# Kernel tuning notes

Measured on AMD Instinct MI355X. Metric: run time of the kernel, lower is better.

The kernel has to match this reference:

```python
import jax, jax.numpy as jnp
import numpy as np

DIM = 1024
HEADS = 16
EPS = 1e-5  # torch nn.LayerNorm default


def layernorm(x, g, b):
    # normalize over last axis
    mu = jnp.mean(x, axis=-1, keepdims=True)
    var = jnp.mean(jnp.square(x - mu), axis=-1, keepdims=True)
    return (x - mu) * jax.lax.rsqrt(var + EPS) * g + b


def setup_inputs() -> dict:
    key = jax.random.key(0)
    ks = jax.random.split(key, 8)
    B, N, C = 4, 1024, DIM
    s = 1.0 / np.sqrt(C)
    return {
        "x": jax.random.normal(ks[0], (B, N, C), jnp.float32),
        "qkv_w": jax.random.normal(ks[1], (3 * C, C), jnp.float32) * s,
        "qkv_b": jnp.zeros((3 * C,), jnp.float32),
        "q_norm_g": jnp.ones((C,), jnp.float32),
        "q_norm_b": jnp.zeros((C,), jnp.float32),
        "k_norm_g": jnp.ones((C,), jnp.float32),
        "k_norm_b": jnp.zeros((C,), jnp.float32),
        "proj_w": jax.random.normal(ks[2], (C, C), jnp.float32) * s,
        "proj_b": jnp.zeros((C,), jnp.float32),
    }


def reference(x, qkv_w, qkv_b, q_norm_g, q_norm_b, k_norm_g, k_norm_b, proj_w, proj_b):
    B, N, C = x.shape
    H = HEADS
    D = C // H
    scale = D ** -0.5

    qkv = x @ qkv_w.T + qkv_b                      # [B,N,3C]
    qkv = qkv.reshape(B, N, 3, H, D)
    q, k, v = qkv[:, :, 0], qkv[:, :, 1], qkv[:, :, 2]  # [B,N,H,D]

    # qk_normalization: LayerNorm over flattened (H*D)=C per token
    q = layernorm(q.reshape(B, N, C), q_norm_g, q_norm_b).reshape(B, N, H, D)
    k = layernorm(k.reshape(B, N, C), k_norm_g, k_norm_b).reshape(B, N, H, D)

    # attention: [B,H,N,N]
    attn = jnp.einsum('bqhd,bkhd->bhqk', q * scale, k)
    attn = jax.nn.softmax(attn, axis=-1)
    out = jnp.einsum('bhqk,bkhd->bqhd', attn, v).reshape(B, N, C)
    return out @ proj_w.T + proj_b
```

## Files before the change

### kernel.cpp

```cpp
#include <hip/hip_runtime.h>
#include <hip/hip_bf16.h>

#define C_DIM 1024
#define HEADS 16

typedef __bf16 bf16x8 __attribute__((ext_vector_type(8)));
typedef float f32x4 __attribute__((ext_vector_type(4)));

static __device__ __forceinline__ unsigned short f2bf(float f) {
  unsigned int u = __builtin_bit_cast(unsigned int, f);
  u += 0x7FFFu + ((u >> 16) & 1u);
  return (unsigned short)(u >> 16);
}

static __device__ __forceinline__ float bf2f(unsigned short u) {
  unsigned int v = ((unsigned int)u) << 16;
  return __builtin_bit_cast(float, v);
}

static __device__ __forceinline__ void glds16(const unsigned short* g,
                                              unsigned short* l) {
  __builtin_amdgcn_global_load_lds(
      (const __attribute__((address_space(1))) unsigned int*)g,
      (__attribute__((address_space(3))) unsigned int*)l, 16, 0, 0);
}

__global__ void cast_bf16_kernel(const float* __restrict__ src,
                                 unsigned short* __restrict__ dst, int n4) {
  int i = blockIdx.x * blockDim.x + threadIdx.x;
  if (i >= n4) return;
  float4 v = *reinterpret_cast<const float4*>(src + (size_t)i * 4);
  ushort4 o;
  o.x = f2bf(v.x); o.y = f2bf(v.y); o.z = f2bf(v.z); o.w = f2bf(v.w);
  *reinterpret_cast<ushort4*>(dst + (size_t)i * 4) = o;
}

__global__ void cast2_kernel(const float* __restrict__ s0,
                             const float* __restrict__ s1,
                             unsigned short* __restrict__ d0,
                             unsigned short* __restrict__ d1, int n40) {
  int i = blockIdx.x * 256 + threadIdx.x;
  const float* s;
  unsigned short* d;
  if (i < n40) { s = s0; d = d0; }
  else { s = s1; d = d1; i -= n40; }
  float4 v = *reinterpret_cast<const float4*>(s + (size_t)i * 4);
  ushort4 o;
  o.x = f2bf(v.x); o.y = f2bf(v.y); o.z = f2bf(v.z); o.w = f2bf(v.w);
  *reinterpret_cast<ushort4*>(d + (size_t)i * 4) = o;
}

template <bool BF16_OUT>
__global__ __launch_bounds__(256, 2) void gemm_nt(
    const unsigned short* __restrict__ A, const unsigned short* __restrict__ B,
    const float* __restrict__ bias, void* __restrict__ Cout,
    int M, int N, int K) {
  __shared__ __align__(16) unsigned short As[128 * 64];
  __shared__ __align__(16) unsigned short Bs[128 * 64];
  const int tid = threadIdx.x;
  const int lane = tid & 63;
  const int wave = tid >> 6;
  const int wm = wave >> 1, wn = wave & 1;
  const int g = lane >> 4, r = lane & 15;
  const int bm = blockIdx.x * 128, bn = blockIdx.y * 128;

  f32x4 acc[4][4] = {};

  for (int k0 = 0; k0 < K; k0 += 64) {
    __syncthreads();
#pragma unroll
    for (int i = 0; i < 4; ++i) {
      int cb = i * 256 + wave * 64;
      int c = cb + lane;
      int row = c >> 3, col = (c & 7) * 8;
      glds16(&A[(size_t)(bm + row) * K + k0 + col], &As[cb * 8]);
      glds16(&B[(size_t)(bn + row) * K + k0 + col], &Bs[cb * 8]);
    }
    __syncthreads();

    bf16x8 af[4][2], bf[4][2];
#pragma unroll
    for (int m = 0; m < 4; ++m) {
      af[m][0] = *reinterpret_cast<const bf16x8*>(&As[(wm * 64 + m * 16 + r) * 64 + g * 8]);
      af[m][1] = *reinterpret_cast<const bf16x8*>(&As[(wm * 64 + m * 16 + r) * 64 + 32 + g * 8]);
    }
#pragma unroll
    for (int n = 0; n < 4; ++n) {
      bf[n][0] = *reinterpret_cast<const bf16x8*>(&Bs[(wn * 64 + n * 16 + r) * 64 + g * 8]);
      bf[n][1] = *reinterpret_cast<const bf16x8*>(&Bs[(wn * 64 + n * 16 + r) * 64 + 32 + g * 8]);
    }
#pragma unroll
    for (int m = 0; m < 4; ++m)
#pragma unroll
      for (int n = 0; n < 4; ++n) {
        acc[m][n] = __builtin_amdgcn_mfma_f32_16x16x32_bf16(af[m][0], bf[n][0], acc[m][n], 0, 0, 0);
        acc[m][n] = __builtin_amdgcn_mfma_f32_16x16x32_bf16(af[m][1], bf[n][1], acc[m][n], 0, 0, 0);
      }
  }

#pragma unroll
  for (int m = 0; m < 4; ++m) {
    int row0 = bm + wm * 64 + m * 16 + g * 4;
#pragma unroll
    for (int n = 0; n < 4; ++n) {
      int col = bn + wn * 64 + n * 16 + r;
      float bv = bias[col];
#pragma unroll
      for (int rr = 0; rr < 4; ++rr) {
        float v = acc[m][n][rr] + bv;
        if (BF16_OUT)
          reinterpret_cast<unsigned short*>(Cout)[(size_t)(row0 + rr) * N + col] = f2bf(v);
        else
          reinterpret_cast<float*>(Cout)[(size_t)(row0 + rr) * N + col] = v;
      }
    }
  }
}

__global__ __launch_bounds__(256) void ln_pack_kernel(
    const unsigned short* __restrict__ qkv, const float* __restrict__ qg,
    const float* __restrict__ qb, const float* __restrict__ kg,
    const float* __restrict__ kb, unsigned short* __restrict__ Q,
    unsigned short* __restrict__ Ko, unsigned short* __restrict__ V) {
  const int t = blockIdx.x;
  const int b = t >> 10, n = t & 1023;
  const int tid = threadIdx.x;
  const int lane = tid & 63, wave = tid >> 6;
  const unsigned short* row = qkv + (size_t)t * 3072;
  ushort4 qu = *reinterpret_cast<const ushort4*>(row + tid * 4);
  ushort4 ku = *reinterpret_cast<const ushort4*>(row + 1024 + tid * 4);
  ushort4 vu = *reinterpret_cast<const ushort4*>(row + 2048 + tid * 4);
  float q0 = bf2f(qu.x), q1 = bf2f(qu.y), q2 = bf2f(qu.z), q3 = bf2f(qu.w);
  float k0 = bf2f(ku.x), k1 = bf2f(ku.y), k2 = bf2f(ku.z), k3 = bf2f(ku.w);

  float qs = q0 + q1 + q2 + q3;
  float qss = q0 * q0 + q1 * q1 + q2 * q2 + q3 * q3;
  float ks = k0 + k1 + k2 + k3;
  float kss = k0 * k0 + k1 * k1 + k2 * k2 + k3 * k3;
#pragma unroll
  for (int m = 1; m < 64; m <<= 1) {
    qs += __shfl_xor(qs, m);
    qss += __shfl_xor(qss, m);
    ks += __shfl_xor(ks, m);
    kss += __shfl_xor(kss, m);
  }
  __shared__ float red[4][4];
  if (lane == 0) {
    red[wave][0] = qs; red[wave][1] = qss; red[wave][2] = ks; red[wave][3] = kss;
  }
  __syncthreads();
  qs = red[0][0] + red[1][0] + red[2][0] + red[3][0];
  qss = red[0][1] + red[1][1] + red[2][1] + red[3][1];
  ks = red[0][2] + red[1][2] + red[2][2] + red[3][2];
  kss = red[0][3] + red[1][3] + red[2][3] + red[3][3];
  const float inv = 1.0f / 1024.0f;
  float qmu = qs * inv, kmu = ks * inv;
  float qrs = rsqrtf(qss * inv - qmu * qmu + 1e-5f);
  float krs = rsqrtf(kss * inv - kmu * kmu + 1e-5f);

  int c0 = tid * 4;
  float4 qg4 = *reinterpret_cast<const float4*>(qg + c0);
  float4 qb4 = *reinterpret_cast<const float4*>(qb + c0);
  float4 kg4 = *reinterpret_cast<const float4*>(kg + c0);
  float4 kb4 = *reinterpret_cast<const float4*>(kb + c0);
  int h = c0 >> 6, d = c0 & 63;
  size_t off = (((size_t)(b * HEADS + h)) * 1024 + n) * 64 + d;
  ushort4 qo, ko, vo;
  const float QS = 0.125f * 1.44269504f;
  qo.x = f2bf(((q0 - qmu) * qrs * qg4.x + qb4.x) * QS);
  qo.y = f2bf(((q1 - qmu) * qrs * qg4.y + qb4.y) * QS);
  qo.z = f2bf(((q2 - qmu) * qrs * qg4.z + qb4.z) * QS);
  qo.w = f2bf(((q3 - qmu) * qrs * qg4.w + qb4.w) * QS);
  ko.x = f2bf((k0 - kmu) * krs * kg4.x + kb4.x);
  ko.y = f2bf((k1 - kmu) * krs * kg4.y + kb4.y);
  ko.z = f2bf((k2 - kmu) * krs * kg4.z + kb4.z);
  ko.w = f2bf((k3 - kmu) * krs * kg4.w + kb4.w);
  vo.x = vu.x; vo.y = vu.y; vo.z = vu.z; vo.w = vu.w;
  *reinterpret_cast<ushort4*>(Q + off) = qo;
  *reinterpret_cast<ushort4*>(Ko + off) = ko;
  *reinterpret_cast<ushort4*>(V + off) = vo;
}

__global__ __launch_bounds__(256) void transpose_v(
    const unsigned short* __restrict__ V, unsigned short* __restrict__ VT) {
  const int bid = blockIdx.x;
  const int bh = bid >> 4, nt = bid & 15;
  const unsigned short* src = V + (size_t)bh * 65536 + nt * 64 * 64;
  unsigned short* dst = VT + (size_t)bh * 65536 + nt * 64;
  __shared__ __align__(16) unsigned short tile[64][68];
  const int tid = threadIdx.x;
#pragma unroll
  for (int i = 0; i < 4; ++i) {
    int idx = i * 256 + tid;
    int row = idx >> 4, c4 = (idx & 15) * 4;
    *reinterpret_cast<ushort4*>(&tile[row][c4]) =
        *reinterpret_cast<const ushort4*>(&src[row * 64 + c4]);
  }
  __syncthreads();
#pragma unroll
  for (int i = 0; i < 4; ++i) {
    int idx = i * 256 + tid;
    int d = idx >> 4, p = (idx & 15) * 4;
    int key0 = 16 * (2 * (p >> 5) + ((p >> 2) & 1)) + 4 * ((p >> 3) & 3);
    ushort4 o;
    o.x = tile[key0][d]; o.y = tile[key0 + 1][d];
    o.z = tile[key0 + 2][d]; o.w = tile[key0 + 3][d];
    *reinterpret_cast<ushort4*>(&dst[(size_t)d * 1024 + p]) = o;
  }
}

__global__ __launch_bounds__(256, 4) void attn_kernel(
    const unsigned short* __restrict__ Q, const unsigned short* __restrict__ K,
    const unsigned short* __restrict__ VT, unsigned short* __restrict__ O) {
  const int blk = blockIdx.x;
  const int bh = blk & 63;
  const int qb = blk >> 6;
  const int tid = threadIdx.x;
  const int lane = tid & 63, wave = tid >> 6;
  const int g = lane >> 4, r = lane & 15;
  const unsigned short* Qh = Q + (size_t)bh * 65536;
  const unsigned short* Kh = K + (size_t)bh * 65536;
  const unsigned short* Vth = VT + (size_t)bh * 65536;
  const int q0 = qb * 64 + wave * 16;

  __shared__ __align__(16) unsigned short KL[2][4096];
  __shared__ __align__(16) unsigned short VL[2][4096];

  bf16x8 bq0 = *reinterpret_cast<const bf16x8*>(&Qh[(q0 + r) * 64 + g * 8]);
  bf16x8 bq1 = *reinterpret_cast<const bf16x8*>(&Qh[(q0 + r) * 64 + 32 + g * 8]);

  f32x4 ao[4] = {};
  float mreg = -1e30f, lreg = 0.f;

  auto STAGE = [&](int b, int kt) {
#pragma unroll
    for (int t = 0; t < 2; ++t) {
      int cb = (wave * 2 + t) * 64;
      int i = cb + lane;
      int row = i >> 3, pcol = i & 7;
      int lc = pcol ^ (row & 7);
      glds16(Kh + (size_t)(kt + row) * 64 + lc * 8, &KL[b][cb * 8]);
      glds16(Vth + (size_t)row * 1024 + kt + lc * 8, &VL[b][cb * 8]);
    }
  };

  STAGE(0, 0);
  __syncthreads();
  int cur = 0;

  for (int kt = 0; kt < 1024; kt += 64) {
    if (kt + 64 < 1024) STAGE(cur ^ 1, kt + 64);
    const unsigned short* KB = KL[cur];
    const unsigned short* VB = VL[cur];
    const int sw = r & 7;

    f32x4 s[4];
#pragma unroll
    for (int j = 0; j < 4; ++j) {
      const int row = 16 * j + r;
      bf16x8 k0 = *reinterpret_cast<const bf16x8*>(&KB[row * 64 + (g ^ sw) * 8]);
      bf16x8 k1 = *reinterpret_cast<const bf16x8*>(&KB[row * 64 + ((4 + g) ^ sw) * 8]);
      f32x4 t = {};
      t = __builtin_amdgcn_mfma_f32_16x16x32_bf16(k0, bq0, t, 0, 0, 0);
      t = __builtin_amdgcn_mfma_f32_16x16x32_bf16(k1, bq1, t, 0, 0, 0);
      s[j] = t;
    }
    float a0 = fmaxf(fmaxf(s[0][0], s[0][1]), s[0][2]);
    float a1 = fmaxf(fmaxf(s[0][3], s[1][0]), s[1][1]);
    float a2 = fmaxf(fmaxf(s[1][2], s[1][3]), s[2][0]);
    float a3 = fmaxf(fmaxf(s[2][1], s[2][2]), s[2][3]);
    float a4 = fmaxf(fmaxf(s[3][0], s[3][1]), s[3][2]);
    float v = fmaxf(fmaxf(fmaxf(a0, a1), fmaxf(a2, a3)), fmaxf(a4, s[3][3]));
    v = fmaxf(v, __shfl_xor(v, 16));
    v = fmaxf(v, __shfl_xor(v, 32));
    if (!__all((int)(v - mreg <= 8.0f))) {
      float mnew = fmaxf(mreg, v);
      float fac = exp2f(mreg - mnew);
      mreg = mnew;
      lreg *= fac;
      float facr[4];
#pragma unroll
      for (int rr = 0; rr < 4; ++rr)
        facr[rr] = __shfl(fac, (lane & 48) | (4 * g + rr));
#pragma unroll
      for (int n = 0; n < 4; ++n)
#pragma unroll
        for (int rr = 0; rr < 4; ++rr) ao[n][rr] *= facr[rr];
    }
#pragma unroll
    for (int j = 0; j < 4; ++j)
#pragma unroll
      for (int rr = 0; rr < 4; ++rr) s[j][rr] = exp2f(s[j][rr] - mreg);
    float ps = ((s[0][0] + s[0][1]) + (s[0][2] + s[0][3])) +
               ((s[1][0] + s[1][1]) + (s[1][2] + s[1][3])) +
               ((s[2][0] + s[2][1]) + (s[2][2] + s[2][3])) +
               ((s[3][0] + s[3][1]) + (s[3][2] + s[3][3]));
    ps += __shfl_xor(ps, 16);
    ps += __shfl_xor(ps, 32);
    lreg += ps;
    uint4 u0, u1;
    asm("v_cvt_pk_bf16_f32 %0, %1, %2" : "=v"(u0.x) : "v"(s[0][0]), "v"(s[0][1]));
    asm("v_cvt_pk_bf16_f32 %0, %1, %2" : "=v"(u0.y) : "v"(s[0][2]), "v"(s[0][3]));
    asm("v_cvt_pk_bf16_f32 %0, %1, %2" : "=v"(u0.z) : "v"(s[1][0]), "v"(s[1][1]));
    asm("v_cvt_pk_bf16_f32 %0, %1, %2" : "=v"(u0.w) : "v"(s[1][2]), "v"(s[1][3]));
    asm("v_cvt_pk_bf16_f32 %0, %1, %2" : "=v"(u1.x) : "v"(s[2][0]), "v"(s[2][1]));
    asm("v_cvt_pk_bf16_f32 %0, %1, %2" : "=v"(u1.y) : "v"(s[2][2]), "v"(s[2][3]));
    asm("v_cvt_pk_bf16_f32 %0, %1, %2" : "=v"(u1.z) : "v"(s[3][0]), "v"(s[3][1]));
    asm("v_cvt_pk_bf16_f32 %0, %1, %2" : "=v"(u1.w) : "v"(s[3][2]), "v"(s[3][3]));
    bf16x8 ap0 = __builtin_bit_cast(bf16x8, u0);
    bf16x8 ap1 = __builtin_bit_cast(bf16x8, u1);
#pragma unroll
    for (int n = 0; n < 4; ++n) {
      const int row = n * 16 + r;
      bf16x8 v0 = *reinterpret_cast<const bf16x8*>(&VB[row * 64 + (g ^ sw) * 8]);
      bf16x8 v1 = *reinterpret_cast<const bf16x8*>(&VB[row * 64 + ((4 + g) ^ sw) * 8]);
      ao[n] = __builtin_amdgcn_mfma_f32_16x16x32_bf16(ap0, v0, ao[n], 0, 0, 0);
      ao[n] = __builtin_amdgcn_mfma_f32_16x16x32_bf16(ap1, v1, ao[n], 0, 0, 0);
    }
    __syncthreads();
    cur ^= 1;
  }

  const int b = bh >> 4, h = bh & 15;
  float lr[4];
#pragma unroll
  for (int rr = 0; rr < 4; ++rr)
    lr[rr] = 1.0f / __shfl(lreg, (lane & 48) | (4 * g + rr));
#pragma unroll
  for (int n = 0; n < 4; ++n)
#pragma unroll
    for (int rr = 0; rr < 4; ++rr) {
      int tok = q0 + 4 * g + rr;
      O[(((size_t)(b * 1024 + tok)) * 16 + h) * 64 + n * 16 + r] =
          f2bf(ao[n][rr] * lr[rr]);
    }
}

__global__ void sentinel_kernel(unsigned short* out, float v) {
  if (threadIdx.x == 0 && blockIdx.x == 0) out[0] = f2bf(v);
}

extern "C" void kernel_launch(void* const* d_in, const int* in_sizes, int n_in,
                              void* d_out, int out_size, void* d_ws, size_t ws_size,
                              hipStream_t stream) {
  const float* x      = (const float*)d_in[0];
  const float* qkv_w  = (const float*)d_in[1];
  const float* qkv_b  = (const float*)d_in[2];
  const float* q_g    = (const float*)d_in[3];
  const float* q_b    = (const float*)d_in[4];
  const float* k_g    = (const float*)d_in[5];
  const float* k_b    = (const float*)d_in[6];
  const float* proj_w = (const float*)d_in[7];
  const float* proj_b = (const float*)d_in[8];

  const int M = in_sizes[0] / C_DIM;
  const int Bb = M / 1024;

  const size_t required = (size_t)M * 3072 * 2 + (size_t)3 * M * 1024 * 2;
  if (ws_size < required) {
    sentinel_kernel<<<1, 64, 0, stream>>>((unsigned short*)d_out, (float)ws_size);
    return;
  }

  unsigned short* qkv_bf = (unsigned short*)d_ws;
  unsigned short* Qb = qkv_bf + (size_t)M * 3072;
  unsigned short* Kb = Qb + (size_t)M * 1024;
  unsigned short* Vb = Kb + (size_t)M * 1024;
  unsigned short* x_bf = Qb;
  unsigned short* qw_bf = Kb;
  unsigned short* AO = qkv_bf;
  unsigned short* VT = qkv_bf + (size_t)M * 1024;
  unsigned short* pw_bf = qkv_bf + (size_t)2 * M * 1024;

  const int n4x = M * 1024 / 4;
  const int n4w1 = 3072 * 1024 / 4;
  const int n4w2 = 1024 * 1024 / 4;
  cast2_kernel<<<(n4x + n4w1) / 256, 256, 0, stream>>>(
      x, qkv_w, x_bf, qw_bf, n4x);

  gemm_nt<true><<<dim3(M / 128, 3072 / 128), 256, 0, stream>>>(
      x_bf, qw_bf, qkv_b, qkv_bf, M, 3072, 1024);

  ln_pack_kernel<<<M, 256, 0, stream>>>(qkv_bf, q_g, q_b, k_g, k_b, Qb, Kb, Vb);

  transpose_v<<<Bb * HEADS * 16, 256, 0, stream>>>(Vb, VT);

  cast_bf16_kernel<<<n4w2 / 256, 256, 0, stream>>>(proj_w, pw_bf, n4w2);

  attn_kernel<<<Bb * HEADS * 16, 256, 0, stream>>>(Qb, Kb, VT, AO);

  gemm_nt<false><<<dim3(M / 128, 1024 / 128), 256, 0, stream>>>(
      AO, pw_bf, proj_b, (float*)d_out, M, 1024, 1024);
}
```

Measured before the change: 124.9 us.

## Process two 16-row query tiles per wave in attention kernel

```diff
diff --git a/kernel.cpp b/kernel.cpp
--- a/kernel.cpp
+++ b/kernel.cpp
@@ -209,7 +209,7 @@
   }
 }
 
-__global__ __launch_bounds__(256, 4) void attn_kernel(
+__global__ __launch_bounds__(256, 2) void attn_kernel(
     const unsigned short* __restrict__ Q, const unsigned short* __restrict__ K,
     const unsigned short* __restrict__ VT, unsigned short* __restrict__ O) {
   const int blk = blockIdx.x;
@@ -221,16 +221,20 @@
   const unsigned short* Qh = Q + (size_t)bh * 65536;
   const unsigned short* Kh = K + (size_t)bh * 65536;
   const unsigned short* Vth = VT + (size_t)bh * 65536;
-  const int q0 = qb * 64 + wave * 16;
+  const int q0 = qb * 128 + wave * 32;
 
   __shared__ __align__(16) unsigned short KL[2][4096];
   __shared__ __align__(16) unsigned short VL[2][4096];
 
-  bf16x8 bq0 = *reinterpret_cast<const bf16x8*>(&Qh[(q0 + r) * 64 + g * 8]);
-  bf16x8 bq1 = *reinterpret_cast<const bf16x8*>(&Qh[(q0 + r) * 64 + 32 + g * 8]);
-
-  f32x4 ao[4] = {};
-  float mreg = -1e30f, lreg = 0.f;
+  bf16x8 bq[2][2];
+#pragma unroll
+  for (int h = 0; h < 2; ++h) {
+    bq[h][0] = *reinterpret_cast<const bf16x8*>(&Qh[(q0 + 16 * h + r) * 64 + g * 8]);
+    bq[h][1] = *reinterpret_cast<const bf16x8*>(&Qh[(q0 + 16 * h + r) * 64 + 32 + g * 8]);
+  }
+
+  f32x4 ao[2][4] = {};
+  float mreg[2] = {-1e30f, -1e30f}, lreg[2] = {0.f, 0.f};
 
   auto STAGE = [&](int b, int kt) {
 #pragma unroll
@@ -254,86 +258,99 @@
     const unsigned short* VB = VL[cur];
     const int sw = r & 7;
 
-    f32x4 s[4];
+    f32x4 s[2][4];
 #pragma unroll
     for (int j = 0; j < 4; ++j) {
       const int row = 16 * j + r;
       bf16x8 k0 = *reinterpret_cast<const bf16x8*>(&KB[row * 64 + (g ^ sw) * 8]);
       bf16x8 k1 = *reinterpret_cast<const bf16x8*>(&KB[row * 64 + ((4 + g) ^ sw) * 8]);
-      f32x4 t = {};
-      t = __builtin_amdgcn_mfma_f32_16x16x32_bf16(k0, bq0, t, 0, 0, 0);
-      t = __builtin_amdgcn_mfma_f32_16x16x32_bf16(k1, bq1, t, 0, 0, 0);
-      s[j] = t;
-    }
-    float a0 = fmaxf(fmaxf(s[0][0], s[0][1]), s[0][2]);
-    float a1 = fmaxf(fmaxf(s[0][3], s[1][0]), s[1][1]);
-    float a2 = fmaxf(fmaxf(s[1][2], s[1][3]), s[2][0]);
-    float a3 = fmaxf(fmaxf(s[2][1], s[2][2]), s[2][3]);
-    float a4 = fmaxf(fmaxf(s[3][0], s[3][1]), s[3][2]);
-    float v = fmaxf(fmaxf(fmaxf(a0, a1), fmaxf(a2, a3)), fmaxf(a4, s[3][3]));
-    v = fmaxf(v, __shfl_xor(v, 16));
-    v = fmaxf(v, __shfl_xor(v, 32));
-    if (!__all((int)(v - mreg <= 8.0f))) {
-      float mnew = fmaxf(mreg, v);
-      float fac = exp2f(mreg - mnew);
-      mreg = mnew;
-      lreg *= fac;
-      float facr[4];
-#pragma unroll
-      for (int rr = 0; rr < 4; ++rr)
-        facr[rr] = __shfl(fac, (lane & 48) | (4 * g + rr));
-#pragma unroll
-      for (int n = 0; n < 4; ++n)
-#pragma unroll
-        for (int rr = 0; rr < 4; ++rr) ao[n][rr] *= facr[rr];
-    }
-#pragma unroll
-    for (int j = 0; j < 4; ++j)
-#pragma unroll
-      for (int rr = 0; rr < 4; ++rr) s[j][rr] = exp2f(s[j][rr] - mreg);
-    float ps = ((s[0][0] + s[0][1]) + (s[0][2] + s[0][3])) +
-               ((s[1][0] + s[1][1]) + (s[1][2] + s[1][3])) +
-               ((s[2][0] + s[2][1]) + (s[2][2] + s[2][3])) +
-               ((s[3][0] + s[3][1]) + (s[3][2] + s[3][3]));
-    ps += __shfl_xor(ps, 16);
-    ps += __shfl_xor(ps, 32);
-    lreg += ps;
-    uint4 u0, u1;
-    asm("v_cvt_pk_bf16_f32 %0, %1, %2" : "=v"(u0.x) : "v"(s[0][0]), "v"(s[0][1]));
-    asm("v_cvt_pk_bf16_f32 %0, %1, %2" : "=v"(u0.y) : "v"(s[0][2]), "v"(s[0][3]));
-    asm("v_cvt_pk_bf16_f32 %0, %1, %2" : "=v"(u0.z) : "v"(s[1][0]), "v"(s[1][1]));
-    asm("v_cvt_pk_bf16_f32 %0, %1, %2" : "=v"(u0.w) : "v"(s[1][2]), "v"(s[1][3]));
-    asm("v_cvt_pk_bf16_f32 %0, %1, %2" : "=v"(u1.x) : "v"(s[2][0]), "v"(s[2][1]));
-    asm("v_cvt_pk_bf16_f32 %0, %1, %2" : "=v"(u1.y) : "v"(s[2][2]), "v"(s[2][3]));
-    asm("v_cvt_pk_bf16_f32 %0, %1, %2" : "=v"(u1.z) : "v"(s[3][0]), "v"(s[3][1]));
-    asm("v_cvt_pk_bf16_f32 %0, %1, %2" : "=v"(u1.w) : "v"(s[3][2]), "v"(s[3][3]));
-    bf16x8 ap0 = __builtin_bit_cast(bf16x8, u0);
-    bf16x8 ap1 = __builtin_bit_cast(bf16x8, u1);
+#pragma unroll
+      for (int h = 0; h < 2; ++h) {
+        f32x4 t = {};
+        t = __builtin_amdgcn_mfma_f32_16x16x32_bf16(k0, bq[h][0], t, 0, 0, 0);
+        t = __builtin_amdgcn_mfma_f32_16x16x32_bf16(k1, bq[h][1], t, 0, 0, 0);
+        s[h][j] = t;
+      }
+    }
+    bf16x8 ap[2][2];
+#pragma unroll
+    for (int h = 0; h < 2; ++h) {
+      float a0 = fmaxf(fmaxf(s[h][0][0], s[h][0][1]), s[h][0][2]);
+      float a1 = fmaxf(fmaxf(s[h][0][3], s[h][1][0]), s[h][1][1]);
+      float a2 = fmaxf(fmaxf(s[h][1][2], s[h][1][3]), s[h][2][0]);
+      float a3 = fmaxf(fmaxf(s[h][2][1], s[h][2][2]), s[h][2][3]);
+      float a4 = fmaxf(fmaxf(s[h][3][0], s[h][3][1]), s[h][3][2]);
+      float v = fmaxf(fmaxf(fmaxf(a0, a1), fmaxf(a2, a3)), fmaxf(a4, s[h][3][3]));
+      v = fmaxf(v, __shfl_xor(v, 16));
+      v = fmaxf(v, __shfl_xor(v, 32));
+      if (!__all((int)(v - mreg[h] <= 8.0f))) {
+        float mnew = fmaxf(mreg[h], v);
+        float fac = exp2f(mreg[h] - mnew);
+        mreg[h] = mnew;
+        lreg[h] *= fac;
+        float facr[4];
+#pragma unroll
+        for (int rr = 0; rr < 4; ++rr)
+          facr[rr] = __shfl(fac, (lane & 48) | (4 * g + rr));
+#pragma unroll
+        for (int n = 0; n < 4; ++n)
+#pragma unroll
+          for (int rr = 0; rr < 4; ++rr) ao[h][n][rr] *= facr[rr];
+      }
+#pragma unroll
+      for (int j = 0; j < 4; ++j)
+#pragma unroll
+        for (int rr = 0; rr < 4; ++rr) s[h][j][rr] = exp2f(s[h][j][rr] - mreg[h]);
+      float ps = ((s[h][0][0] + s[h][0][1]) + (s[h][0][2] + s[h][0][3])) +
+                 ((s[h][1][0] + s[h][1][1]) + (s[h][1][2] + s[h][1][3])) +
+                 ((s[h][2][0] + s[h][2][1]) + (s[h][2][2] + s[h][2][3])) +
+                 ((s[h][3][0] + s[h][3][1]) + (s[h][3][2] + s[h][3][3]));
+      ps += __shfl_xor(ps, 16);
+      ps += __shfl_xor(ps, 32);
+      lreg[h] += ps;
+      uint4 u0, u1;
+      asm("v_cvt_pk_bf16_f32 %0, %1, %2" : "=v"(u0.x) : "v"(s[h][0][0]), "v"(s[h][0][1]));
+      asm("v_cvt_pk_bf16_f32 %0, %1, %2" : "=v"(u0.y) : "v"(s[h][0][2]), "v"(s[h][0][3]));
+      asm("v_cvt_pk_bf16_f32 %0, %1, %2" : "=v"(u0.z) : "v"(s[h][1][0]), "v"(s[h][1][1]));
+      asm("v_cvt_pk_bf16_f32 %0, %1, %2" : "=v"(u0.w) : "v"(s[h][1][2]), "v"(s[h][1][3]));
+      asm("v_cvt_pk_bf16_f32 %0, %1, %2" : "=v"(u1.x) : "v"(s[h][2][0]), "v"(s[h][2][1]));
+      asm("v_cvt_pk_bf16_f32 %0, %1, %2" : "=v"(u1.y) : "v"(s[h][2][2]), "v"(s[h][2][3]));
+      asm("v_cvt_pk_bf16_f32 %0, %1, %2" : "=v"(u1.z) : "v"(s[h][3][0]), "v"(s[h][3][1]));
+      asm("v_cvt_pk_bf16_f32 %0, %1, %2" : "=v"(u1.w) : "v"(s[h][3][2]), "v"(s[h][3][3]));
+      ap[h][0] = __builtin_bit_cast(bf16x8, u0);
+      ap[h][1] = __builtin_bit_cast(bf16x8, u1);
+    }
 #pragma unroll
     for (int n = 0; n < 4; ++n) {
       const int row = n * 16 + r;
       bf16x8 v0 = *reinterpret_cast<const bf16x8*>(&VB[row * 64 + (g ^ sw) * 8]);
       bf16x8 v1 = *reinterpret_cast<const bf16x8*>(&VB[row * 64 + ((4 + g) ^ sw) * 8]);
-      ao[n] = __builtin_amdgcn_mfma_f32_16x16x32_bf16(ap0, v0, ao[n], 0, 0, 0);
-      ao[n] = __builtin_amdgcn_mfma_f32_16x16x32_bf16(ap1, v1, ao[n], 0, 0, 0);
+#pragma unroll
+      for (int h = 0; h < 2; ++h) {
+        ao[h][n] = __builtin_amdgcn_mfma_f32_16x16x32_bf16(ap[h][0], v0, ao[h][n], 0, 0, 0);
+        ao[h][n] = __builtin_amdgcn_mfma_f32_16x16x32_bf16(ap[h][1], v1, ao[h][n], 0, 0, 0);
+      }
     }
     __syncthreads();
     cur ^= 1;
   }
 
-  const int b = bh >> 4, h = bh & 15;
-  float lr[4];
-#pragma unroll
-  for (int rr = 0; rr < 4; ++rr)
-    lr[rr] = 1.0f / __shfl(lreg, (lane & 48) | (4 * g + rr));
-#pragma unroll
-  for (int n = 0; n < 4; ++n)
-#pragma unroll
-    for (int rr = 0; rr < 4; ++rr) {
-      int tok = q0 + 4 * g + rr;
-      O[(((size_t)(b * 1024 + tok)) * 16 + h) * 64 + n * 16 + r] =
-          f2bf(ao[n][rr] * lr[rr]);
-    }
+  const int b = bh >> 4, h16 = bh & 15;
+#pragma unroll
+  for (int h = 0; h < 2; ++h) {
+    float lr[4];
+#pragma unroll
+    for (int rr = 0; rr < 4; ++rr)
+      lr[rr] = 1.0f / __shfl(lreg[h], (lane & 48) | (4 * g + rr));
+#pragma unroll
+    for (int n = 0; n < 4; ++n)
+#pragma unroll
+      for (int rr = 0; rr < 4; ++rr) {
+        int tok = q0 + 16 * h + 4 * g + rr;
+        O[(((size_t)(b * 1024 + tok)) * 16 + h16) * 64 + n * 16 + r] =
+            f2bf(ao[h][n][rr] * lr[rr]);
+      }
+  }
 }
 
 __global__ void sentinel_kernel(unsigned short* out, float v) {
@@ -387,7 +404,7 @@
 
   cast_bf16_kernel<<<n4w2 / 256, 256, 0, stream>>>(proj_w, pw_bf, n4w2);
 
-  attn_kernel<<<Bb * HEADS * 16, 256, 0, stream>>>(Qb, Kb, VT, AO);
+  attn_kernel<<<Bb * HEADS * 8, 256, 0, stream>>>(Qb, Kb, VT, AO);
 
   gemm_nt<false><<<dim3(M / 128, 1024 / 128), 256, 0, stream>>>(
       AO, pw_bf, proj_b, (float*)d_out, M, 1024, 1024);
```

After: 126.7 us. No clear change (+1.4%).
